# Kernel optimization log

Hardware: AMD Instinct MI355X
Metric: run time of the kernel (lower is better)

## Reference

```python
import jax, jax.numpy as jnp
import numpy as np
from jax import lax

NUM_INPUTS = 1024
NUM_OUTPUTS = 1024
NUM_LAYERS = 32          # 1 first + (NUM_LAYERS-1) middle + 1 last, per torch __init__
N = 4096                 # num_neurons_per_layer
W = 65536                # parallel bit-array width


def _nand_layer(x, idx, mask):
    # x: [num_in, W] bool; idx: [num_out, 2] int; mask: [num_out] bool
    g = x[idx]                       # [num_out, 2, W] gather
    out = g[:, 0, :] & g[:, 1, :]    # bitwise AND
    return jnp.where(mask[:, None], ~out, out)  # conditional NOT


def setup_inputs() -> dict:
    key = jax.random.key(0)
    k = jax.random.split(key, 7)
    n_mid = NUM_LAYERS - 1
    return {
        "input_bitarrays": jax.random.bernoulli(k[0], 0.5, (NUM_INPUTS, W)),
        "idx_first": jax.random.randint(k[1], (N, 2), 0, NUM_INPUTS, dtype=jnp.int64 if jax.config.jax_enable_x64 else jnp.int32),
        "mask_first": jax.random.bernoulli(k[2], 0.5, (N,)),
        "idx_mid": jax.random.randint(k[3], (n_mid, N, 2), 0, N, dtype=jnp.int64 if jax.config.jax_enable_x64 else jnp.int32),
        "mask_mid": jax.random.bernoulli(k[4], 0.5, (n_mid, N)),
        "idx_last": jax.random.randint(k[5], (NUM_OUTPUTS, 2), 0, N, dtype=jnp.int64 if jax.config.jax_enable_x64 else jnp.int32),
        "mask_last": jax.random.bernoulli(k[6], 0.5, (NUM_OUTPUTS,)),
    }


def reference(input_bitarrays, idx_first, mask_first, idx_mid, mask_mid, idx_last, mask_last):
    x = _nand_layer(input_bitarrays, idx_first, mask_first)

    def step(carry, params):
        idx, mask = params
        return _nand_layer(carry, idx, mask), None

    x, _ = lax.scan(step, x, (idx_mid, mask_mid))
    return _nand_layer(x, idx_last, mask_last)
```

## Files before the change

kernel.cpp:

```cpp
#include <hip/hip_runtime.h>
#include <stdint.h>

#define NINPUTS   1024
#define NOUTPUTS  1024
#define NMID      31
#define NN        4096
#define W         65536
#define CHUNK     128
#define WPN       4
#define NCHUNKS   (W / CHUNK)
#define GRID      256
#define CPW       (NCHUNKS / GRID)
#define THREADS   1024
#define NPAIRS    16
#define TBL_BYTES ((size_t)NPAIRS * NN * 16)

#define LIGHT_BARRIER() asm volatile("s_waitcnt lgkmcnt(0)\n\ts_barrier" ::: "memory")

__global__ void build_tbl_kernel(const int*      __restrict__ idx_first,
                                 const uint32_t* __restrict__ mask_first,
                                 const int*      __restrict__ idx_mid,
                                 const uint32_t* __restrict__ mask_mid,
                                 uint4*          __restrict__ tbl)
{
    const int tid = blockIdx.x * blockDim.x + threadIdx.x;
    const int F = tid >> 12;
    const int n = tid & (NN - 1);

    const int*      i1;
    const uint32_t* m1;
    if (F == 0) { i1 = idx_first; m1 = mask_first; }
    else        { i1 = idx_mid + (size_t)(2 * F - 1) * NN * 2;
                  m1 = mask_mid + (size_t)(2 * F - 1) * NN; }
    const int*      i2 = idx_mid + (size_t)(2 * F) * NN * 2;
    const uint32_t* m2 = mask_mid + (size_t)(2 * F) * NN;

    const int j = i2[2 * n];
    const int k = i2[2 * n + 1];
    uint4 e;
    e.x = (uint32_t)(i1[2 * j]     * 16) | (m1[j] ? 0x80000000u : 0u);
    e.y = (uint32_t)(i1[2 * j + 1] * 16);
    e.z = (uint32_t)(i1[2 * k]     * 16) | (m1[k] ? 0x80000000u : 0u);
    e.w = (uint32_t)(i1[2 * k + 1] * 16) | (m2[n] ? 0x80000000u : 0u);
    tbl[(size_t)F * NN + n] = e;
}

__global__ __launch_bounds__(THREADS, 4)
void nand_fused_kernel(const uint32_t* __restrict__ in,
                       const uint4*    __restrict__ tbl,
                       const int*      __restrict__ idx_last,
                       const uint32_t* __restrict__ mask_last,
                       uint32_t*       __restrict__ out)
{
    __shared__ uint32_t lds[40960];
    uint32_t* P = lds;
    uint32_t* X = lds + 4096;
    uint32_t* Y = lds + 20480;
    uint32_t* R = lds + 36864;

    const int t      = threadIdx.x;
    const int l      = t & 63;
    const int wv     = t >> 6;
    const int lane32 = l & 31;
    const int half   = l >> 5;
    const int shift  = half ? 32 : 0;
    const int bcol   = blockIdx.x * (CPW * CHUNK);

    #pragma unroll 4
    for (int s = 0; s < 32; ++s) {
        const int r = s * 32 + wv * 2 + half;
        const uint4 v = *(const uint4*)(in + (size_t)r * W + bcol + lane32 * 4);
        const unsigned long long b0 = __ballot(v.x != 0u);
        const unsigned long long b1 = __ballot(v.y != 0u);
        const unsigned long long b2 = __ballot(v.z != 0u);
        const unsigned long long b3 = __ballot(v.w != 0u);
        if (lane32 == 0) {
            uint4 w;
            w.x = (uint32_t)(b0 >> shift);
            w.y = (uint32_t)(b1 >> shift);
            w.z = (uint32_t)(b2 >> shift);
            w.w = (uint32_t)(b3 >> shift);
            *(uint4*)&P[r * WPN] = w;
        }
    }
    __syncthreads();

    for (int i = 0; i < CPW; ++i) {
        const int c0n = bcol + (i + 1) * CHUNK;
        const int c0p = bcol + (i - 1) * CHUNK;
        const bool do_pack   = (i + 1 < CPW);
        const bool do_unpack = (i > 0);

        uint4 tc[4], tn[4];
        #pragma unroll
        for (int k = 0; k < 4; ++k) tc[k] = tbl[k * THREADS + t];

        for (int F = 0; F <= 16; ++F) {
            uint4 pv0 = {0,0,0,0}, pv1 = {0,0,0,0};
            int pr0 = 0, pr1 = 0;
            if (do_pack && F >= 1) {
                pr0 = (F - 1) * 64 + wv * 2 + half;
                pr1 = pr0 + 32;
                pv0 = *(const uint4*)(in + (size_t)pr0 * W + c0n + lane32 * 4);
                pv1 = *(const uint4*)(in + (size_t)pr1 * W + c0n + lane32 * 4);
            }

            if (F <= 15) {
                const uint32_t* src = (F == 0) ? P : ((F & 1) ? X : Y);
                uint32_t*       dst = (F & 1) ? Y : X;
                uint4 A[4], B[4], C[4], D[4];
                #pragma unroll
                for (int k = 0; k < 4; ++k) {
                    const uint4 e = tc[k];
                    A[k] = *(const uint4*)((const char*)src + (e.x & 0xFFFFu));
                    B[k] = *(const uint4*)((const char*)src + e.y);
                    C[k] = *(const uint4*)((const char*)src + (e.z & 0xFFFFu));
                    D[k] = *(const uint4*)((const char*)src + (e.w & 0xFFFFu));
                }
                #pragma unroll
                for (int k = 0; k < 4; ++k) {
                    const int n = k * THREADS + t;
                    const uint4 e = tc[k];
                    const uint32_t xm1 = (uint32_t)((int32_t)e.x >> 31);
                    const uint32_t xm2 = (uint32_t)((int32_t)e.z >> 31);
                    const uint32_t xm3 = (uint32_t)((int32_t)e.w >> 31);
                    uint4 r;
                    r.x = (((A[k].x & B[k].x) ^ xm1) & ((C[k].x & D[k].x) ^ xm2)) ^ xm3;
                    r.y = (((A[k].y & B[k].y) ^ xm1) & ((C[k].y & D[k].y) ^ xm2)) ^ xm3;
                    r.z = (((A[k].z & B[k].z) ^ xm1) & ((C[k].z & D[k].z) ^ xm2)) ^ xm3;
                    r.w = (((A[k].w & B[k].w) ^ xm1) & ((C[k].w & D[k].w) ^ xm2)) ^ xm3;
                    *(uint4*)&dst[n * WPN] = r;
                }
            } else {
                const int n = t;
                const int2 ij = ((const int2*)idx_last)[n];
                const uint32_t xm = mask_last[n] ? 0xFFFFFFFFu : 0u;
                const uint4 a = *(const uint4*)&Y[ij.x * WPN];
                const uint4 b = *(const uint4*)&Y[ij.y * WPN];
                uint4 r;
                r.x = (a.x & b.x) ^ xm;  r.y = (a.y & b.y) ^ xm;
                r.z = (a.z & b.z) ^ xm;  r.w = (a.w & b.w) ^ xm;
                *(uint4*)&R[n * WPN] = r;
            }

            if (F <= 14) {
                #pragma unroll
                for (int k = 0; k < 4; ++k)
                    tn[k] = tbl[(size_t)(F + 1) * NN + k * THREADS + t];
            }

            if (do_unpack && F <= 15) {
                #pragma unroll
                for (int s = 0; s < 2; ++s) {
                    const int r = F * 64 + s * 32 + wv * 2 + half;
                    const uint4 w4 = *(const uint4*)&R[r * WPN];
                    uint4 v;
                    v.x = (w4.x >> lane32) & 1u;
                    v.y = (w4.y >> lane32) & 1u;
                    v.z = (w4.z >> lane32) & 1u;
                    v.w = (w4.w >> lane32) & 1u;
                    *(uint4*)(out + (size_t)r * W + c0p + lane32 * 4) = v;
                }
            }

            if (do_pack && F >= 1) {
                {
                    const unsigned long long b0 = __ballot(pv0.x != 0u);
                    const unsigned long long b1 = __ballot(pv0.y != 0u);
                    const unsigned long long b2 = __ballot(pv0.z != 0u);
                    const unsigned long long b3 = __ballot(pv0.w != 0u);
                    if (lane32 == 0) {
                        uint4 w;
                        w.x = (uint32_t)(b0 >> shift);
                        w.y = (uint32_t)(b1 >> shift);
                        w.z = (uint32_t)(b2 >> shift);
                        w.w = (uint32_t)(b3 >> shift);
                        *(uint4*)&P[pr0 * WPN] = w;
                    }
                }
                {
                    const unsigned long long b0 = __ballot(pv1.x != 0u);
                    const unsigned long long b1 = __ballot(pv1.y != 0u);
                    const unsigned long long b2 = __ballot(pv1.z != 0u);
                    const unsigned long long b3 = __ballot(pv1.w != 0u);
                    if (lane32 == 0) {
                        uint4 w;
                        w.x = (uint32_t)(b0 >> shift);
                        w.y = (uint32_t)(b1 >> shift);
                        w.z = (uint32_t)(b2 >> shift);
                        w.w = (uint32_t)(b3 >> shift);
                        *(uint4*)&P[pr1 * WPN] = w;
                    }
                }
            }

            if (F <= 14) {
                #pragma unroll
                for (int k = 0; k < 4; ++k) tc[k] = tn[k];
            }
            LIGHT_BARRIER();
        }
    }

    {
        const int c0l = bcol + (CPW - 1) * CHUNK;
        #pragma unroll 4
        for (int s = 0; s < 32; ++s) {
            const int r = s * 32 + wv * 2 + half;
            const uint4 w4 = *(const uint4*)&R[r * WPN];
            uint4 v;
            v.x = (w4.x >> lane32) & 1u;
            v.y = (w4.y >> lane32) & 1u;
            v.z = (w4.z >> lane32) & 1u;
            v.w = (w4.w >> lane32) & 1u;
            *(uint4*)(out + (size_t)r * W + c0l + lane32 * 4) = v;
        }
    }
}

__global__ __launch_bounds__(THREADS, 4)
void nand_pipe128_kernel(const uint32_t* __restrict__ in,
                         const int*      __restrict__ idx_first,
                         const uint32_t* __restrict__ mask_first,
                         const int*      __restrict__ idx_mid,
                         const uint32_t* __restrict__ mask_mid,
                         const int*      __restrict__ idx_last,
                         const uint32_t* __restrict__ mask_last,
                         uint32_t*       __restrict__ out)
{
    __shared__ uint32_t lds[40960];
    uint32_t* P = lds;
    uint32_t* X = lds + 4096;
    uint32_t* Y = lds + 20480;
    uint32_t* R = lds + 36864;

    const int t      = threadIdx.x;
    const int l      = t & 63;
    const int wv     = t >> 6;
    const int lane32 = l & 31;
    const int half   = l >> 5;
    const int shift  = half ? 32 : 0;
    const int bcol   = blockIdx.x * (CPW * CHUNK);

    #pragma unroll 4
    for (int s = 0; s < 32; ++s) {
        const int r = s * 32 + wv * 2 + half;
        const uint4 v = *(const uint4*)(in + (size_t)r * W + bcol + lane32 * 4);
        const unsigned long long b0 = __ballot(v.x != 0u);
        const unsigned long long b1 = __ballot(v.y != 0u);
        const unsigned long long b2 = __ballot(v.z != 0u);
        const unsigned long long b3 = __ballot(v.w != 0u);
        if (lane32 == 0) {
            uint4 w;
            w.x = (uint32_t)(b0 >> shift);  w.y = (uint32_t)(b1 >> shift);
            w.z = (uint32_t)(b2 >> shift);  w.w = (uint32_t)(b3 >> shift);
            *(uint4*)&P[r * WPN] = w;
        }
    }
    __syncthreads();

    for (int i = 0; i < CPW; ++i) {
        const int c0n = bcol + (i + 1) * CHUNK;
        const int c0p = bcol + (i - 1) * CHUNK;
        const bool do_pack   = (i + 1 < CPW);
        const bool do_unpack = (i > 0);

        for (int L = 0; L <= 32; ++L) {
            uint4 pv = {0, 0, 0, 0};
            int   pr = 0;
            if (do_pack && L >= 1) {
                pr = (L - 1) * 32 + wv * 2 + half;
                pv = *(const uint4*)(in + (size_t)pr * W + c0n + lane32 * 4);
            }
            if (L == 0) {
                #pragma unroll
                for (int k = 0; k < NN / THREADS; ++k) {
                    const int n = k * THREADS + t;
                    const int2 ij = ((const int2*)idx_first)[n];
                    const uint32_t xm = mask_first[n] ? 0xFFFFFFFFu : 0u;
                    const uint4 a = *(const uint4*)&P[ij.x * WPN];
                    const uint4 b = *(const uint4*)&P[ij.y * WPN];
                    uint4 r;
                    r.x = (a.x & b.x) ^ xm;  r.y = (a.y & b.y) ^ xm;
                    r.z = (a.z & b.z) ^ xm;  r.w = (a.w & b.w) ^ xm;
                    *(uint4*)&X[n * WPN] = r;
                }
            } else if (L <= 31) {
                const int*      idxL = idx_mid + (size_t)(L - 1) * NN * 2;
                const uint32_t* mL   = mask_mid + (size_t)(L - 1) * NN;
                const uint32_t* src  = (L & 1) ? X : Y;
                uint32_t*       dst  = (L & 1) ? Y : X;
                #pragma unroll
                for (int k = 0; k < NN / THREADS; ++k) {
                    const int n = k * THREADS + t;
                    const int2 ij = ((const int2*)idxL)[n];
                    const uint32_t xm = mL[n] ? 0xFFFFFFFFu : 0u;
                    const uint4 a = *(const uint4*)&src[ij.x * WPN];
                    const uint4 b = *(const uint4*)&src[ij.y * WPN];
                    uint4 r;
                    r.x = (a.x & b.x) ^ xm;  r.y = (a.y & b.y) ^ xm;
                    r.z = (a.z & b.z) ^ xm;  r.w = (a.w & b.w) ^ xm;
                    *(uint4*)&dst[n * WPN] = r;
                }
            } else {
                const int n = t;
                const int2 ij = ((const int2*)idx_last)[n];
                const uint32_t xm = mask_last[n] ? 0xFFFFFFFFu : 0u;
                const uint4 a = *(const uint4*)&Y[ij.x * WPN];
                const uint4 b = *(const uint4*)&Y[ij.y * WPN];
                uint4 r;
                r.x = (a.x & b.x) ^ xm;  r.y = (a.y & b.y) ^ xm;
                r.z = (a.z & b.z) ^ xm;  r.w = (a.w & b.w) ^ xm;
                *(uint4*)&R[n * WPN] = r;
            }
            if (do_unpack && L <= 31) {
                const int r = L * 32 + wv * 2 + half;
                const uint4 w4 = *(const uint4*)&R[r * WPN];
                uint4 v;
                v.x = (w4.x >> lane32) & 1u;  v.y = (w4.y >> lane32) & 1u;
                v.z = (w4.z >> lane32) & 1u;  v.w = (w4.w >> lane32) & 1u;
                *(uint4*)(out + (size_t)r * W + c0p + lane32 * 4) = v;
            }
            if (do_pack && L >= 1) {
                const unsigned long long b0 = __ballot(pv.x != 0u);
                const unsigned long long b1 = __ballot(pv.y != 0u);
                const unsigned long long b2 = __ballot(pv.z != 0u);
                const unsigned long long b3 = __ballot(pv.w != 0u);
                if (lane32 == 0) {
                    uint4 w;
                    w.x = (uint32_t)(b0 >> shift);  w.y = (uint32_t)(b1 >> shift);
                    w.z = (uint32_t)(b2 >> shift);  w.w = (uint32_t)(b3 >> shift);
                    *(uint4*)&P[pr * WPN] = w;
                }
            }
            __syncthreads();
        }
    }
    {
        const int c0l = bcol + (CPW - 1) * CHUNK;
        #pragma unroll 4
        for (int s = 0; s < 32; ++s) {
            const int r = s * 32 + wv * 2 + half;
            const uint4 w4 = *(const uint4*)&R[r * WPN];
            uint4 v;
            v.x = (w4.x >> lane32) & 1u;  v.y = (w4.y >> lane32) & 1u;
            v.z = (w4.z >> lane32) & 1u;  v.w = (w4.w >> lane32) & 1u;
            *(uint4*)(out + (size_t)r * W + c0l + lane32 * 4) = v;
        }
    }
}

extern "C" void kernel_launch(void* const* d_in, const int* in_sizes, int n_in,
                              void* d_out, int out_size, void* d_ws, size_t ws_size,
                              hipStream_t stream) {
    const uint32_t* in         = (const uint32_t*)d_in[0];
    const int*      idx_first  = (const int*)d_in[1];
    const uint32_t* mask_first = (const uint32_t*)d_in[2];
    const int*      idx_mid    = (const int*)d_in[3];
    const uint32_t* mask_mid   = (const uint32_t*)d_in[4];
    const int*      idx_last   = (const int*)d_in[5];
    const uint32_t* mask_last  = (const uint32_t*)d_in[6];
    uint32_t*       out        = (uint32_t*)d_out;

    if (ws_size >= TBL_BYTES) {
        uint4* tbl = (uint4*)d_ws;
        build_tbl_kernel<<<(NPAIRS * NN) / 256, 256, 0, stream>>>(
            idx_first, mask_first, idx_mid, mask_mid, tbl);
        nand_fused_kernel<<<GRID, THREADS, 0, stream>>>(
            in, tbl, idx_last, mask_last, out);
    } else {
        nand_pipe128_kernel<<<GRID, THREADS, 0, stream>>>(
            in, idx_first, mask_first, idx_mid, mask_mid, idx_last, mask_last, out);
    }
}
```

Before: 152.5 us.

## Halve chunk width, use SoA LDS layout with ds_read2st64, double grid

Reduces per-block chunk from 128 to 64 columns and doubles the grid to 512 blocks. Intermediate node bits move to a structure-of-arrays LDS layout accessed with ds_read2st64/ds_write2st64, so each gather takes one instruction for two words. This halves LDS use per block to allow more blocks per CU. Blocks are remapped so that paired chunks share an XCD, and the table prefetch into registers is replaced by a load at each step. More blocks and barriers add scheduling overhead, and the per-step table loads are no longer hidden behind compute.

```diff
diff --git a/kernel.cpp b/kernel.cpp
--- a/kernel.cpp
+++ b/kernel.cpp
@@ -6,14 +6,25 @@
 #define NMID      31
 #define NN        4096
 #define W         65536
-#define CHUNK     128
-#define WPN       4
+#define CHUNK     64
 #define NCHUNKS   (W / CHUNK)
-#define GRID      256
+#define GRID      512
 #define CPW       (NCHUNKS / GRID)
 #define THREADS   1024
 #define NPAIRS    16
 #define TBL_BYTES ((size_t)NPAIRS * NN * 16)
+
+#define PB  0u
+#define X0B 8192u
+#define Y0B 40960u
+#define RB  73728u
+
+#define SOA_READ2(DST, VA)                                                   \
+    asm volatile("ds_read2st64_b32 %0, %1 offset0:0 offset1:64"              \
+                 : "=v"(DST) : "v"(VA))
+#define SOA_WRITE2(VA, LO, HI)                                               \
+    asm volatile("ds_write2st64_b32 %0, %1, %2 offset0:0 offset1:64"         \
+                 :: "v"(VA), "v"(LO), "v"(HI))
 
 #define LIGHT_BARRIER() asm volatile("s_waitcnt lgkmcnt(0)\n\ts_barrier" ::: "memory")
 
@@ -35,88 +46,83 @@
     const int*      i2 = idx_mid + (size_t)(2 * F) * NN * 2;
     const uint32_t* m2 = mask_mid + (size_t)(2 * F) * NN;
 
+    const uint32_t scale = (F == 0) ? 8u : 4u;
     const int j = i2[2 * n];
     const int k = i2[2 * n + 1];
     uint4 e;
-    e.x = (uint32_t)(i1[2 * j]     * 16) | (m1[j] ? 0x80000000u : 0u);
-    e.y = (uint32_t)(i1[2 * j + 1] * 16);
-    e.z = (uint32_t)(i1[2 * k]     * 16) | (m1[k] ? 0x80000000u : 0u);
-    e.w = (uint32_t)(i1[2 * k + 1] * 16) | (m2[n] ? 0x80000000u : 0u);
+    e.x = (uint32_t)i1[2 * j]     * scale | (m1[j] ? 0x80000000u : 0u);
+    e.y = (uint32_t)i1[2 * j + 1] * scale;
+    e.z = (uint32_t)i1[2 * k]     * scale | (m1[k] ? 0x80000000u : 0u);
+    e.w = (uint32_t)i1[2 * k + 1] * scale | (m2[n] ? 0x80000000u : 0u);
     tbl[(size_t)F * NN + n] = e;
 }
 
-__global__ __launch_bounds__(THREADS, 4)
+__global__ __launch_bounds__(THREADS, 8)
 void nand_fused_kernel(const uint32_t* __restrict__ in,
                        const uint4*    __restrict__ tbl,
                        const int*      __restrict__ idx_last,
                        const uint32_t* __restrict__ mask_last,
                        uint32_t*       __restrict__ out)
 {
-    __shared__ uint32_t lds[40960];
+    __shared__ uint32_t lds[20480];
     uint32_t* P = lds;
-    uint32_t* X = lds + 4096;
-    uint32_t* Y = lds + 20480;
-    uint32_t* R = lds + 36864;
-
-    const int t      = threadIdx.x;
-    const int l      = t & 63;
-    const int wv     = t >> 6;
+    uint32_t* R = lds + (RB / 4);
+
+    const int t  = threadIdx.x;
+    const int l  = t & 63;
+    const int wv = t >> 6;
     const int lane32 = l & 31;
-    const int half   = l >> 5;
-    const int shift  = half ? 32 : 0;
-    const int bcol   = blockIdx.x * (CPW * CHUNK);
-
-    #pragma unroll 4
-    for (int s = 0; s < 32; ++s) {
-        const int r = s * 32 + wv * 2 + half;
-        const uint4 v = *(const uint4*)(in + (size_t)r * W + bcol + lane32 * 4);
-        const unsigned long long b0 = __ballot(v.x != 0u);
-        const unsigned long long b1 = __ballot(v.y != 0u);
-        const unsigned long long b2 = __ballot(v.z != 0u);
-        const unsigned long long b3 = __ballot(v.w != 0u);
-        if (lane32 == 0) {
-            uint4 w;
-            w.x = (uint32_t)(b0 >> shift);
-            w.y = (uint32_t)(b1 >> shift);
-            w.z = (uint32_t)(b2 >> shift);
-            w.w = (uint32_t)(b3 >> shift);
-            *(uint4*)&P[r * WPN] = w;
+
+    const int b      = blockIdx.x;
+    const int xcd    = b & 7;
+    const int jj     = b >> 4;
+    const int hh     = (b >> 3) & 1;
+    const int pairid = xcd * 32 + jj;
+    const int chunk0 = 2 * pairid + hh;
+
+    {
+        const int c0 = chunk0 * CHUNK;
+        #pragma unroll 4
+        for (int s = 0; s < 16; ++s) {
+            #pragma unroll
+            for (int q = 0; q < 4; ++q) {
+                const int r = s * 64 + wv * 4 + q;
+                const uint32_t v = in[(size_t)r * W + c0 + l];
+                const unsigned long long bb = __ballot(v != 0u);
+                if (l == 0) {
+                    uint2 w;
+                    w.x = (uint32_t)bb;
+                    w.y = (uint32_t)(bb >> 32);
+                    *(uint2*)&P[r * 2] = w;
+                }
+            }
         }
     }
     __syncthreads();
 
     for (int i = 0; i < CPW; ++i) {
-        const int c0n = bcol + (i + 1) * CHUNK;
-        const int c0p = bcol + (i - 1) * CHUNK;
+        const int c0n = (chunk0 + 512 * (i + 1)) * CHUNK;
+        const int c0p = (chunk0 + 512 * (i - 1)) * CHUNK;
         const bool do_pack   = (i + 1 < CPW);
         const bool do_unpack = (i > 0);
 
-        uint4 tc[4], tn[4];
-        #pragma unroll
-        for (int k = 0; k < 4; ++k) tc[k] = tbl[k * THREADS + t];
-
         for (int F = 0; F <= 16; ++F) {
-            uint4 pv0 = {0,0,0,0}, pv1 = {0,0,0,0};
-            int pr0 = 0, pr1 = 0;
+            uint32_t pv[4];
+            int prow = 0;
             if (do_pack && F >= 1) {
-                pr0 = (F - 1) * 64 + wv * 2 + half;
-                pr1 = pr0 + 32;
-                pv0 = *(const uint4*)(in + (size_t)pr0 * W + c0n + lane32 * 4);
-                pv1 = *(const uint4*)(in + (size_t)pr1 * W + c0n + lane32 * 4);
-            }
-
+                prow = (F - 1) * 64 + wv * 4;
+                #pragma unroll
+                for (int q = 0; q < 4; ++q)
+                    pv[q] = in[(size_t)(prow + q) * W + c0n + l];
+            }
+            uint4 tc[4];
             if (F <= 15) {
-                const uint32_t* src = (F == 0) ? P : ((F & 1) ? X : Y);
-                uint32_t*       dst = (F & 1) ? Y : X;
-                uint4 A[4], B[4], C[4], D[4];
-                #pragma unroll
-                for (int k = 0; k < 4; ++k) {
-                    const uint4 e = tc[k];
-                    A[k] = *(const uint4*)((const char*)src + (e.x & 0xFFFFu));
-                    B[k] = *(const uint4*)((const char*)src + e.y);
-                    C[k] = *(const uint4*)((const char*)src + (e.z & 0xFFFFu));
-                    D[k] = *(const uint4*)((const char*)src + (e.w & 0xFFFFu));
-                }
+                #pragma unroll
+                for (int k = 0; k < 4; ++k)
+                    tc[k] = tbl[(size_t)F * NN + k * THREADS + t];
+            }
+
+            if (F == 0) {
                 #pragma unroll
                 for (int k = 0; k < 4; ++k) {
                     const int n = k * THREADS + t;
@@ -124,100 +130,102 @@
                     const uint32_t xm1 = (uint32_t)((int32_t)e.x >> 31);
                     const uint32_t xm2 = (uint32_t)((int32_t)e.z >> 31);
                     const uint32_t xm3 = (uint32_t)((int32_t)e.w >> 31);
-                    uint4 r;
-                    r.x = (((A[k].x & B[k].x) ^ xm1) & ((C[k].x & D[k].x) ^ xm2)) ^ xm3;
-                    r.y = (((A[k].y & B[k].y) ^ xm1) & ((C[k].y & D[k].y) ^ xm2)) ^ xm3;
-                    r.z = (((A[k].z & B[k].z) ^ xm1) & ((C[k].z & D[k].z) ^ xm2)) ^ xm3;
-                    r.w = (((A[k].w & B[k].w) ^ xm1) & ((C[k].w & D[k].w) ^ xm2)) ^ xm3;
-                    *(uint4*)&dst[n * WPN] = r;
+                    const uint2 a = *(const uint2*)((const char*)lds + PB + (e.x & 0xFFFFu));
+                    const uint2 bb = *(const uint2*)((const char*)lds + PB + e.y);
+                    const uint2 c = *(const uint2*)((const char*)lds + PB + (e.z & 0xFFFFu));
+                    const uint2 d = *(const uint2*)((const char*)lds + PB + (e.w & 0xFFFFu));
+                    const uint32_t r0 = (((a.x & bb.x) ^ xm1) & ((c.x & d.x) ^ xm2)) ^ xm3;
+                    const uint32_t r1 = (((a.y & bb.y) ^ xm1) & ((c.y & d.y) ^ xm2)) ^ xm3;
+                    SOA_WRITE2(X0B + (uint32_t)n * 4u, r0, r1);
+                }
+            } else if (F <= 15) {
+                const uint32_t sb0 = (F & 1) ? X0B : Y0B;
+                const uint32_t db0 = (F & 1) ? Y0B : X0B;
+                uint64_t A[4], B[4], C[4], D[4];
+                #pragma unroll
+                for (int k = 0; k < 4; ++k) {
+                    const uint4 e = tc[k];
+                    SOA_READ2(A[k], sb0 + (e.x & 0xFFFFu));
+                    SOA_READ2(B[k], sb0 + e.y);
+                    SOA_READ2(C[k], sb0 + (e.z & 0xFFFFu));
+                    SOA_READ2(D[k], sb0 + (e.w & 0xFFFFu));
+                }
+                asm volatile("s_waitcnt lgkmcnt(0)" ::: "memory");
+                __builtin_amdgcn_sched_barrier(0);
+                #pragma unroll
+                for (int k = 0; k < 4; ++k) {
+                    const int n = k * THREADS + t;
+                    const uint4 e = tc[k];
+                    const uint32_t xm1 = (uint32_t)((int32_t)e.x >> 31);
+                    const uint32_t xm2 = (uint32_t)((int32_t)e.z >> 31);
+                    const uint32_t xm3 = (uint32_t)((int32_t)e.w >> 31);
+                    const uint32_t r0 = ((((uint32_t)A[k] & (uint32_t)B[k]) ^ xm1) &
+                                         (((uint32_t)C[k] & (uint32_t)D[k]) ^ xm2)) ^ xm3;
+                    const uint32_t r1 = ((((uint32_t)(A[k] >> 32) & (uint32_t)(B[k] >> 32)) ^ xm1) &
+                                         (((uint32_t)(C[k] >> 32) & (uint32_t)(D[k] >> 32)) ^ xm2)) ^ xm3;
+                    SOA_WRITE2(db0 + (uint32_t)n * 4u, r0, r1);
                 }
             } else {
                 const int n = t;
                 const int2 ij = ((const int2*)idx_last)[n];
                 const uint32_t xm = mask_last[n] ? 0xFFFFFFFFu : 0u;
-                const uint4 a = *(const uint4*)&Y[ij.x * WPN];
-                const uint4 b = *(const uint4*)&Y[ij.y * WPN];
-                uint4 r;
-                r.x = (a.x & b.x) ^ xm;  r.y = (a.y & b.y) ^ xm;
-                r.z = (a.z & b.z) ^ xm;  r.w = (a.w & b.w) ^ xm;
-                *(uint4*)&R[n * WPN] = r;
-            }
-
-            if (F <= 14) {
-                #pragma unroll
-                for (int k = 0; k < 4; ++k)
-                    tn[k] = tbl[(size_t)(F + 1) * NN + k * THREADS + t];
+                uint64_t a, bb;
+                SOA_READ2(a,  Y0B + (uint32_t)ij.x * 4u);
+                SOA_READ2(bb, Y0B + (uint32_t)ij.y * 4u);
+                asm volatile("s_waitcnt lgkmcnt(0)" ::: "memory");
+                __builtin_amdgcn_sched_barrier(0);
+                uint2 r;
+                r.x = ((uint32_t)a         & (uint32_t)bb)         ^ xm;
+                r.y = ((uint32_t)(a >> 32) & (uint32_t)(bb >> 32)) ^ xm;
+                *(uint2*)&R[n * 2] = r;
             }
 
             if (do_unpack && F <= 15) {
-                #pragma unroll
-                for (int s = 0; s < 2; ++s) {
-                    const int r = F * 64 + s * 32 + wv * 2 + half;
-                    const uint4 w4 = *(const uint4*)&R[r * WPN];
-                    uint4 v;
-                    v.x = (w4.x >> lane32) & 1u;
-                    v.y = (w4.y >> lane32) & 1u;
-                    v.z = (w4.z >> lane32) & 1u;
-                    v.w = (w4.w >> lane32) & 1u;
-                    *(uint4*)(out + (size_t)r * W + c0p + lane32 * 4) = v;
+                const int ur = F * 64 + wv * 4;
+                #pragma unroll
+                for (int q = 0; q < 4; ++q) {
+                    const uint2 w = *(const uint2*)&R[(ur + q) * 2];
+                    const uint32_t sel = (l < 32) ? w.x : w.y;
+                    out[(size_t)(ur + q) * W + c0p + l] = (sel >> lane32) & 1u;
                 }
             }
 
             if (do_pack && F >= 1) {
-                {
-                    const unsigned long long b0 = __ballot(pv0.x != 0u);
-                    const unsigned long long b1 = __ballot(pv0.y != 0u);
-                    const unsigned long long b2 = __ballot(pv0.z != 0u);
-                    const unsigned long long b3 = __ballot(pv0.w != 0u);
-                    if (lane32 == 0) {
-                        uint4 w;
-                        w.x = (uint32_t)(b0 >> shift);
-                        w.y = (uint32_t)(b1 >> shift);
-                        w.z = (uint32_t)(b2 >> shift);
-                        w.w = (uint32_t)(b3 >> shift);
-                        *(uint4*)&P[pr0 * WPN] = w;
+                #pragma unroll
+                for (int q = 0; q < 4; ++q) {
+                    const unsigned long long bb = __ballot(pv[q] != 0u);
+                    if (l == 0) {
+                        uint2 w;
+                        w.x = (uint32_t)bb;
+                        w.y = (uint32_t)(bb >> 32);
+                        *(uint2*)&P[(prow + q) * 2] = w;
                     }
                 }
-                {
-                    const unsigned long long b0 = __ballot(pv1.x != 0u);
-                    const unsigned long long b1 = __ballot(pv1.y != 0u);
-                    const unsigned long long b2 = __ballot(pv1.z != 0u);
-                    const unsigned long long b3 = __ballot(pv1.w != 0u);
-                    if (lane32 == 0) {
-                        uint4 w;
-                        w.x = (uint32_t)(b0 >> shift);
-                        w.y = (uint32_t)(b1 >> shift);
-                        w.z = (uint32_t)(b2 >> shift);
-                        w.w = (uint32_t)(b3 >> shift);
-                        *(uint4*)&P[pr1 * WPN] = w;
-                    }
-                }
-            }
-
-            if (F <= 14) {
-                #pragma unroll
-                for (int k = 0; k < 4; ++k) tc[k] = tn[k];
-            }
+            }
+
             LIGHT_BARRIER();
         }
     }
 
     {
-        const int c0l = bcol + (CPW - 1) * CHUNK;
+        const int c0l = (chunk0 + 512 * (CPW - 1)) * CHUNK;
         #pragma unroll 4
-        for (int s = 0; s < 32; ++s) {
-            const int r = s * 32 + wv * 2 + half;
-            const uint4 w4 = *(const uint4*)&R[r * WPN];
-            uint4 v;
-            v.x = (w4.x >> lane32) & 1u;
-            v.y = (w4.y >> lane32) & 1u;
-            v.z = (w4.z >> lane32) & 1u;
-            v.w = (w4.w >> lane32) & 1u;
-            *(uint4*)(out + (size_t)r * W + c0l + lane32 * 4) = v;
+        for (int s = 0; s < 16; ++s) {
+            #pragma unroll
+            for (int q = 0; q < 4; ++q) {
+                const int r = s * 64 + wv * 4 + q;
+                const uint2 w = *(const uint2*)&R[r * 2];
+                const uint32_t sel = (l < 32) ? w.x : w.y;
+                out[(size_t)r * W + c0l + l] = (sel >> lane32) & 1u;
+            }
         }
     }
 }
 
+#define FCHUNK  128
+#define FWPN    4
+#define FGRID   256
+#define FCPW    2
 __global__ __launch_bounds__(THREADS, 4)
 void nand_pipe128_kernel(const uint32_t* __restrict__ in,
                          const int*      __restrict__ idx_first,
@@ -240,7 +248,7 @@
     const int lane32 = l & 31;
     const int half   = l >> 5;
     const int shift  = half ? 32 : 0;
-    const int bcol   = blockIdx.x * (CPW * CHUNK);
+    const int bcol   = blockIdx.x * (FCPW * FCHUNK);
 
     #pragma unroll 4
     for (int s = 0; s < 32; ++s) {
@@ -254,15 +262,15 @@
             uint4 w;
             w.x = (uint32_t)(b0 >> shift);  w.y = (uint32_t)(b1 >> shift);
             w.z = (uint32_t)(b2 >> shift);  w.w = (uint32_t)(b3 >> shift);
-            *(uint4*)&P[r * WPN] = w;
+            *(uint4*)&P[r * FWPN] = w;
         }
     }
     __syncthreads();
 
-    for (int i = 0; i < CPW; ++i) {
-        const int c0n = bcol + (i + 1) * CHUNK;
-        const int c0p = bcol + (i - 1) * CHUNK;
-        const bool do_pack   = (i + 1 < CPW);
+    for (int i = 0; i < FCPW; ++i) {
+        const int c0n = bcol + (i + 1) * FCHUNK;
+        const int c0p = bcol + (i - 1) * FCHUNK;
+        const bool do_pack   = (i + 1 < FCPW);
         const bool do_unpack = (i > 0);
 
         for (int L = 0; L <= 32; ++L) {
@@ -278,12 +286,12 @@
                     const int n = k * THREADS + t;
                     const int2 ij = ((const int2*)idx_first)[n];
                     const uint32_t xm = mask_first[n] ? 0xFFFFFFFFu : 0u;
-                    const uint4 a = *(const uint4*)&P[ij.x * WPN];
-                    const uint4 b = *(const uint4*)&P[ij.y * WPN];
+                    const uint4 a = *(const uint4*)&P[ij.x * FWPN];
+                    const uint4 b = *(const uint4*)&P[ij.y * FWPN];
                     uint4 r;
                     r.x = (a.x & b.x) ^ xm;  r.y = (a.y & b.y) ^ xm;
                     r.z = (a.z & b.z) ^ xm;  r.w = (a.w & b.w) ^ xm;
-                    *(uint4*)&X[n * WPN] = r;
+                    *(uint4*)&X[n * FWPN] = r;
                 }
             } else if (L <= 31) {
                 const int*      idxL = idx_mid + (size_t)(L - 1) * NN * 2;
@@ -295,27 +303,27 @@
                     const int n = k * THREADS + t;
                     const int2 ij = ((const int2*)idxL)[n];
                     const uint32_t xm = mL[n] ? 0xFFFFFFFFu : 0u;
-                    const uint4 a = *(const uint4*)&src[ij.x * WPN];
-                    const uint4 b = *(const uint4*)&src[ij.y * WPN];
+                    const uint4 a = *(const uint4*)&src[ij.x * FWPN];
+                    const uint4 b = *(const uint4*)&src[ij.y * FWPN];
                     uint4 r;
                     r.x = (a.x & b.x) ^ xm;  r.y = (a.y & b.y) ^ xm;
                     r.z = (a.z & b.z) ^ xm;  r.w = (a.w & b.w) ^ xm;
-                    *(uint4*)&dst[n * WPN] = r;
+                    *(uint4*)&dst[n * FWPN] = r;
                 }
             } else {
                 const int n = t;
                 const int2 ij = ((const int2*)idx_last)[n];
                 const uint32_t xm = mask_last[n] ? 0xFFFFFFFFu : 0u;
-                const uint4 a = *(const uint4*)&Y[ij.x * WPN];
-                const uint4 b = *(const uint4*)&Y[ij.y * WPN];
+                const uint4 a = *(const uint4*)&Y[ij.x * FWPN];
+                const uint4 b = *(const uint4*)&Y[ij.y * FWPN];
                 uint4 r;
                 r.x = (a.x & b.x) ^ xm;  r.y = (a.y & b.y) ^ xm;
                 r.z = (a.z & b.z) ^ xm;  r.w = (a.w & b.w) ^ xm;
-                *(uint4*)&R[n * WPN] = r;
+                *(uint4*)&R[n * FWPN] = r;
             }
             if (do_unpack && L <= 31) {
                 const int r = L * 32 + wv * 2 + half;
-                const uint4 w4 = *(const uint4*)&R[r * WPN];
+                const uint4 w4 = *(const uint4*)&R[r * FWPN];
                 uint4 v;
                 v.x = (w4.x >> lane32) & 1u;  v.y = (w4.y >> lane32) & 1u;
                 v.z = (w4.z >> lane32) & 1u;  v.w = (w4.w >> lane32) & 1u;
@@ -330,18 +338,18 @@
                     uint4 w;
                     w.x = (uint32_t)(b0 >> shift);  w.y = (uint32_t)(b1 >> shift);
                     w.z = (uint32_t)(b2 >> shift);  w.w = (uint32_t)(b3 >> shift);
-                    *(uint4*)&P[pr * WPN] = w;
+                    *(uint4*)&P[pr * FWPN] = w;
                 }
             }
             __syncthreads();
         }
     }
     {
-        const int c0l = bcol + (CPW - 1) * CHUNK;
+        const int c0l = bcol + (FCPW - 1) * FCHUNK;
         #pragma unroll 4
         for (int s = 0; s < 32; ++s) {
             const int r = s * 32 + wv * 2 + half;
-            const uint4 w4 = *(const uint4*)&R[r * WPN];
+            const uint4 w4 = *(const uint4*)&R[r * FWPN];
             uint4 v;
             v.x = (w4.x >> lane32) & 1u;  v.y = (w4.y >> lane32) & 1u;
             v.z = (w4.z >> lane32) & 1u;  v.w = (w4.w >> lane32) & 1u;
@@ -369,7 +377,7 @@
         nand_fused_kernel<<<GRID, THREADS, 0, stream>>>(
             in, tbl, idx_last, mask_last, out);
     } else {
-        nand_pipe128_kernel<<<GRID, THREADS, 0, stream>>>(
+        nand_pipe128_kernel<<<FGRID, THREADS, 0, stream>>>(
             in, idx_first, mask_first, idx_mid, mask_mid, idx_last, mask_last, out);
     }
 }
```

Result: slower. 211.4 us (+38.6%).
